# Optimization experiments

Measured on AMD Instinct MI355X. Metric: run time of the kernel, lower is better.

The kernel has to match this reference:

```python
import jax, jax.numpy as jnp
import numpy as np

B, L, D, H, PD = 4, 8192, 512, 8, 1
DK = D // H
EPS = 1e-5


def setup_inputs() -> dict:
    root = jax.random.key(0)
    ks = jax.random.split(root, 16)
    s = 0.02
    inp = {
        'query': jax.random.normal(ks[0], (B, L, D), jnp.float32),
        'key': jax.random.normal(ks[1], (B, L, D), jnp.float32),
        'value': jax.random.normal(ks[2], (B, L, D), jnp.float32),
        'pos': jax.random.uniform(ks[3], (B, L, PD), jnp.float32),
        # QKV projections (xavier-ish small + diagonal init, as in _reset_parameters)
        'Wq': s * jax.random.normal(ks[4], (D, D), jnp.float32) + 0.01 * jnp.eye(D),
        'bq': jnp.zeros((D,), jnp.float32),
        'Wk': s * jax.random.normal(ks[5], (D, D), jnp.float32) + 0.01 * jnp.eye(D),
        'bk': jnp.zeros((D,), jnp.float32),
        'Wv': s * jax.random.normal(ks[6], (D, D), jnp.float32) + 0.01 * jnp.eye(D),
        'bv': jnp.zeros((D,), jnp.float32),
        # per-head LayerNorm affine params for K and V: [H, DK]
        'gK': jnp.ones((H, DK), jnp.float32),
        'betaK': jnp.zeros((H, DK), jnp.float32),
        'gV': jnp.ones((H, DK), jnp.float32),
        'betaV': jnp.zeros((H, DK), jnp.float32),
        # output fc: (D + H*PD) -> D
        'fcW': s * jax.random.normal(ks[7], (D, D + H * PD), jnp.float32),
        'fcb': jnp.zeros((D,), jnp.float32),
    }
    return inp


def _proj(x, W, b):
    # [B,L,D] -> [B,H,L,DK]
    return (x @ W.T + b).reshape(B, L, H, DK).transpose(0, 2, 1, 3)


def _head_layernorm(x, g, b):
    # x: [B,H,L,DK]; per-head affine params g,b: [H,DK]; biased variance (torch LN)
    m = x.mean(-1, keepdims=True)
    v = x.var(-1, keepdims=True)
    xn = (x - m) * jax.lax.rsqrt(v + EPS)
    return xn * g[None, :, None, :] + b[None, :, None, :]


def reference(query, key, value, pos, Wq, bq, Wk, bk, Wv, bv,
              gK, betaK, gV, betaV, fcW, fcb):
    q = _proj(query, Wq, bq)
    k = _proj(key, Wk, bk)
    v = _proj(value, Wv, bv)
    k = _head_layernorm(k, gK, betaK)
    v = _head_layernorm(v, gV, betaV)
    # positional concat: pos [B,L,PD] -> [B,H,L,PD], concat on feature dim
    p = jnp.broadcast_to(pos[:, None, :, :], (B, H, L, PD))
    q = jnp.concatenate([p, q], axis=-1)  # [B,H,L,DK+PD]
    k = jnp.concatenate([p, k], axis=-1)
    v = jnp.concatenate([p, v], axis=-1)
    # Galerkin linear attention: (K^T V)/L then Q @ that
    attn = jnp.einsum('bhld,bhle->bhde', k, v) / L  # [B,H,DK+PD,DK+PD]
    out = jnp.einsum('bhld,bhde->bhle', q, attn)    # [B,H,L,DK+PD]
    out = out.transpose(0, 2, 1, 3).reshape(B, L, H * (DK + PD))
    att_output = out @ fcW.T + fcb  # [B,L,D]
    return (att_output, attn)
```

## Files before the change

kernel.cpp:

```cpp
#include <hip/hip_runtime.h>

typedef __attribute__((ext_vector_type(8))) short short8;
typedef __attribute__((ext_vector_type(4))) float f32x4;
typedef __attribute__((ext_vector_type(4))) unsigned int uint4v;
typedef unsigned short ushort;
typedef unsigned int uint;

#define B_  4
#define L_  8192
#define D_  512
#define H_  8
#define F_  65
#define KVS_ 80
#define EPS_ 1e-5f

__device__ __forceinline__ ushort f2b(float f) {
    uint x = __float_as_uint(f);
    uint r = (x + 0x7FFFu + ((x >> 16) & 1u)) >> 16;
    return (ushort)r;
}
__device__ __forceinline__ float b2f(ushort u) {
    return __uint_as_float(((uint)u) << 16);
}

#define GLD16(gptr, sptr) \
    __builtin_amdgcn_global_load_lds((const __attribute__((address_space(1))) void*)(gptr), \
                                     (__attribute__((address_space(3))) void*)(sptr), 16, 0, 0)


__global__ __launch_bounds__(256)
void cast_w(const float* __restrict__ Wk, const float* __restrict__ Wv,
            ushort* __restrict__ Wb)
{
    const int g = blockIdx.x * 256 + threadIdx.x;
    const int inner = g & 511;
    const int tileIdx = g >> 9;
    const int w   = inner >> 7;
    const int row = inner & 127;
    const int ks  = tileIdx & 15;
    const int nt  = (tileIdx >> 4) & 3;
    const int z   = tileIdx >> 6;
    const float* __restrict__ src = (z == 0) ? Wk : Wv;
    const float* s = &src[(size_t)(nt * 128 + row) * D_ + ks * 32 + w * 8];
    const float4 f0 = *(const float4*)s;
    const float4 f1 = *(const float4*)(s + 4);
    short8 v;
    v[0] = (short)f2b(f0.x); v[1] = (short)f2b(f0.y);
    v[2] = (short)f2b(f0.z); v[3] = (short)f2b(f0.w);
    v[4] = (short)f2b(f1.x); v[5] = (short)f2b(f1.y);
    v[6] = (short)f2b(f1.z); v[7] = (short)f2b(f1.w);
    *(short8*)&Wb[(size_t)tileIdx * 4096 + inner * 8] = v;
}

__global__ __launch_bounds__(512, 2)
void proj_mfma(const float* __restrict__ Xk, const float* __restrict__ Xv,
               const ushort* __restrict__ Wb,
               const float* __restrict__ bk, const float* __restrict__ bv,
               const float* __restrict__ pos,
               const float* __restrict__ gK, const float* __restrict__ betaK,
               const float* __restrict__ gV, const float* __restrict__ betaV,
               ushort* __restrict__ Kh, ushort* __restrict__ Vh)
{
    const int x  = blockIdx.x;
    const int m0 = ((x & 7) * 32 + (x >> 3)) * 128;
    const int z  = blockIdx.y;

    const float* __restrict__ X    = (z == 0) ? Xk : Xv;
    const float* __restrict__ bias = (z == 0) ? bk : bv;

    const int t  = threadIdx.x;
    const int w  = t >> 6, l = t & 63;
    const int wm = (w >> 2) * 64, wn = (w & 3) * 128;
    const int lg = l >> 4, lm = l & 15;

    __shared__ __align__(16) float sAf[2][4096];
    __shared__ __align__(16) short sB[2][16384];

    f32x4 acc[4][8];
#pragma unroll
    for (int i = 0; i < 4; ++i)
#pragma unroll
        for (int j = 0; j < 8; ++j) acc[i][j] = (f32x4){0.f, 0.f, 0.f, 0.f};

    const int lr = l >> 3;
    const int hg = (l & 7) ^ lr;
    const float* ag[2]; int alo[2];
#pragma unroll
    for (int i = 0; i < 2; ++i) {
        const int row = w * 16 + i * 8 + lr;
        ag[i]  = &X[(size_t)(m0 + row) * D_ + hg * 4];
        alo[i] = (w * 2 + i) * 256;
    }

    const ushort* bsrc[4];
#pragma unroll
    for (int nt = 0; nt < 4; ++nt)
        bsrc[nt] = Wb + (size_t)((z * 4 + nt) * 16) * 4096 + t * 8;

    int a0o[4], a1o[4], bro[8];
#pragma unroll
    for (int i = 0; i < 4; ++i) {
        const int r = wm + i * 16 + lm;
        a0o[i] = r * 32 + (((lg * 2)     ^ (r & 7)) * 4);
        a1o[i] = r * 32 + (((lg * 2 + 1) ^ (r & 7)) * 4);
    }
#pragma unroll
    for (int i = 0; i < 8; ++i) {
        const int col = wn + i * 16 + lm;
        bro[i] = (col >> 7) * 4096 + lg * 1024 + (col & 127) * 8;
    }

    auto stage = [&](int ks, int buf) {
#pragma unroll
        for (int i = 0; i < 2; ++i) GLD16(ag[i] + ks * 32, &sAf[buf][alo[i]]);
#pragma unroll
        for (int nt = 0; nt < 4; ++nt)
            GLD16(bsrc[nt] + (size_t)ks * 4096, &sB[buf][nt * 4096 + t * 8]);
    };

    stage(0, 0);
    int cur = 0;
#pragma unroll
    for (int ks = 0; ks < 16; ++ks) {
        __syncthreads();
        if (ks < 15) stage(ks + 1, cur ^ 1);

        short8 af[4], bfv[8];
#pragma unroll
        for (int i = 0; i < 4; ++i) {
            const f32x4 A0 = *(const f32x4*)&sAf[cur][a0o[i]];
            const f32x4 A1 = *(const f32x4*)&sAf[cur][a1o[i]];
            uint u0, u1, u2, u3;
            asm("v_cvt_pk_bf16_f32 %0, %1, %2" : "=v"(u0) : "v"(A0[0]), "v"(A0[1]));
            asm("v_cvt_pk_bf16_f32 %0, %1, %2" : "=v"(u1) : "v"(A0[2]), "v"(A0[3]));
            asm("v_cvt_pk_bf16_f32 %0, %1, %2" : "=v"(u2) : "v"(A1[0]), "v"(A1[1]));
            asm("v_cvt_pk_bf16_f32 %0, %1, %2" : "=v"(u3) : "v"(A1[2]), "v"(A1[3]));
            union { uint4v u4; short8 s8; } cv;
            cv.u4 = (uint4v){u0, u1, u2, u3};
            af[i] = cv.s8;
        }
#pragma unroll
        for (int i = 0; i < 8; ++i) bfv[i] = *(const short8*)&sB[cur][bro[i]];
#pragma unroll
        for (int mt = 0; mt < 4; ++mt)
#pragma unroll
            for (int nt = 0; nt < 8; ++nt)
                acc[mt][nt] = __builtin_amdgcn_mfma_f32_16x16x32_bf16(
                    af[mt], bfv[nt], acc[mt][nt], 0, 0, 0);

        cur ^= 1;
    }

    const int h0 = wn >> 6;
    float bvv[8];
#pragma unroll
    for (int nt = 0; nt < 8; ++nt) bvv[nt] = bias[wn + nt * 16 + lm];

    const float* gp = (z == 0) ? gK : gV;
    const float* bp = (z == 0) ? betaK : betaV;
    ushort* Oh = (z == 0) ? Kh : Vh;
    float gg[8], bb2[8];
#pragma unroll
    for (int nt = 0; nt < 8; ++nt) {
        const int idx = (h0 + (nt >> 2)) * 64 + (nt & 3) * 16 + lm;
        gg[nt]  = gp[idx];
        bb2[nt] = bp[idx];
    }
#pragma unroll
    for (int mt = 0; mt < 4; ++mt) {
#pragma unroll
        for (int r = 0; r < 4; ++r) {
            const int m = m0 + wm + mt * 16 + lg * 4 + r;
            const int bb = m >> 13, ll = m & 8191;
#pragma unroll
            for (int g = 0; g < 2; ++g) {
                const float v0 = acc[mt][g * 4 + 0][r] + bvv[g * 4 + 0];
                const float v1 = acc[mt][g * 4 + 1][r] + bvv[g * 4 + 1];
                const float v2 = acc[mt][g * 4 + 2][r] + bvv[g * 4 + 2];
                const float v3 = acc[mt][g * 4 + 3][r] + bvv[g * 4 + 3];
                float s = v0 + v1 + v2 + v3;
                float q = v0 * v0 + v1 * v1 + v2 * v2 + v3 * v3;
                s += __shfl_xor(s, 1); s += __shfl_xor(s, 2);
                s += __shfl_xor(s, 4); s += __shfl_xor(s, 8);
                q += __shfl_xor(q, 1); q += __shfl_xor(q, 2);
                q += __shfl_xor(q, 4); q += __shfl_xor(q, 8);
                const float mean = s * (1.f / 64.f);
                const float var = q * (1.f / 64.f) - mean * mean;
                const float rs = rsqrtf(var + EPS_);
                const int h = h0 + g;
                ushort* row = Oh + ((size_t)(bb * H_ + h) * L_ + ll) * KVS_;
                row[1 + 0 * 16 + lm] = f2b((v0 - mean) * rs * gg[g * 4 + 0] + bb2[g * 4 + 0]);
                row[1 + 1 * 16 + lm] = f2b((v1 - mean) * rs * gg[g * 4 + 1] + bb2[g * 4 + 1]);
                row[1 + 2 * 16 + lm] = f2b((v2 - mean) * rs * gg[g * 4 + 2] + bb2[g * 4 + 2]);
                row[1 + 3 * 16 + lm] = f2b((v3 - mean) * rs * gg[g * 4 + 3] + bb2[g * 4 + 3]);
                if (lm == 15) row[0] = f2b(pos[m]);
                else          row[F_ + lm] = 0;
            }
        }
    }
}

__global__ __launch_bounds__(256)
void attn_accum(const ushort* __restrict__ Kh, const ushort* __restrict__ Vh,
                float* __restrict__ attn_acc)
{
    const int s = blockIdx.x;
    const int h = blockIdx.y;
    const int b = blockIdx.z;
    const int t = threadIdx.x;

    __shared__ __align__(16) float Ks[64][84];
    __shared__ __align__(16) float Vs[64][84];

    const size_t base = ((size_t)(b * H_ + h) * L_ + s * 512) * KVS_;

    float acc[5][5];
#pragma unroll
    for (int i = 0; i < 5; ++i)
#pragma unroll
        for (int j = 0; j < 5; ++j) acc[i][j] = 0.f;

    const int dg = t / 13, eg = t % 13;
    const bool act = (t < 169);
    const int d0 = dg * 5, e0 = eg * 5;

    for (int c = 0; c < 8; ++c) {
#pragma unroll
        for (int i = 0; i < 3; ++i) {
            const int slot = t + i * 256;
            if (slot < 640) {
                const int r = slot / 10;
                const int cc = (slot - r * 10) * 8;
                const size_t g = base + (size_t)(c * 64 + r) * KVS_ + cc;
                const short8 kv = *(const short8*)(const void*)&Kh[g];
                const short8 vv = *(const short8*)(const void*)&Vh[g];
                float* kd = &Ks[r][cc];
                float* vd = &Vs[r][cc];
#pragma unroll
                for (int e = 0; e < 8; ++e) {
                    kd[e] = b2f((ushort)kv[e]);
                    vd[e] = b2f((ushort)vv[e]);
                }
            }
        }
        __syncthreads();
        if (act) {
#pragma unroll 2
            for (int l = 0; l < 64; ++l) {
                float kf[5], vf[5];
#pragma unroll
                for (int i = 0; i < 5; ++i) kf[i] = Ks[l][d0 + i];
#pragma unroll
                for (int j = 0; j < 5; ++j) vf[j] = Vs[l][e0 + j];
#pragma unroll
                for (int i = 0; i < 5; ++i)
#pragma unroll
                    for (int j = 0; j < 5; ++j)
                        acc[i][j] = fmaf(kf[i], vf[j], acc[i][j]);
            }
        }
        __syncthreads();
    }

    if (act) {
        float* dst = attn_acc + (size_t)(b * H_ + h) * (F_ * F_);
#pragma unroll
        for (int i = 0; i < 5; ++i)
#pragma unroll
            for (int j = 0; j < 5; ++j)
                atomicAdd(&dst[(d0 + i) * F_ + (e0 + j)], acc[i][j]);
    }
}

__global__ __launch_bounds__(256)
void attn_fin(const float* __restrict__ attn_acc, const float* __restrict__ fcW,
              float* __restrict__ attn_out, float* __restrict__ Gq,
              float* __restrict__ gt0)
{
    const int nc = blockIdx.x;
    const int h = blockIdx.y;
    const int b = blockIdx.z;
    const int t = threadIdx.x;

    __shared__ float S[F_][F_];
    __shared__ float Wl[64][F_];

    const float inv = 1.0f / (float)L_;
    const float* __restrict__ src = attn_acc + (size_t)(b * H_ + h) * F_ * F_;
    for (int idx = t; idx < F_ * F_; idx += 256) {
        const float v = src[idx] * inv;
        S[idx / F_][idx % F_] = v;
        if (nc == 0) attn_out[(size_t)(b * H_ + h) * F_ * F_ + idx] = v;
    }
    for (int idx = t; idx < 64 * F_; idx += 256) {
        const int j = idx / F_;
        const int e = idx - j * F_;
        Wl[j][e] = fcW[(size_t)(nc * 64 + j) * (H_ * F_) + h * F_ + e];
    }
    __syncthreads();

    for (int idx = t; idx < F_ * 64; idx += 256) {
        const int d = idx >> 6;
        const int j = idx & 63;
        float g = 0.f;
#pragma unroll 5
        for (int e = 0; e < F_; ++e) g = fmaf(S[d][e], Wl[j][e], g);
        const int n = nc * 64 + j;
        if (d == 0) gt0[((size_t)b * 512 + n) * 8 + h] = g;
        else        Gq[((size_t)b * 512 + n) * 512 + h * 64 + (d - 1)] = g;
    }
}

__global__ __launch_bounds__(256)
void w2_build(const float* __restrict__ Gq, const float* __restrict__ gt0,
              const float* __restrict__ Wq, const float* __restrict__ bq,
              const float* __restrict__ fcb, ushort* __restrict__ W2pk,
              float* __restrict__ Pv, float* __restrict__ C2v)
{
    const int kt  = blockIdx.x;
    const int ntb = blockIdx.y;
    const int b   = blockIdx.z;
    const int t   = threadIdx.x;
    const int n0 = ntb * 64, k0 = kt * 64;

    __shared__ float Sg[64][65];
    __shared__ float Sw[64][65];

    const float* __restrict__ gq = Gq + (size_t)b * 262144;

    float acc[4][4];
#pragma unroll
    for (int i = 0; i < 4; ++i)
#pragma unroll
        for (int j = 0; j < 4; ++j) acc[i][j] = 0.f;
    float c2a[4] = {0.f, 0.f, 0.f, 0.f};

    const int tn = t >> 4, tk = t & 15;

    for (int dc = 0; dc < 8; ++dc) {
        const int d0 = dc * 64;
        for (int idx = t; idx < 4096; idx += 256) {
            const int rr = idx >> 6, cc = idx & 63;
            Sg[rr][cc] = gq[(size_t)(n0 + rr) * 512 + d0 + cc];
            Sw[rr][cc] = Wq[(size_t)(d0 + rr) * 512 + k0 + cc];
        }
        __syncthreads();
        for (int dd = 0; dd < 64; ++dd) {
            float gf[4], wf[4];
#pragma unroll
            for (int i = 0; i < 4; ++i) gf[i] = Sg[tn * 4 + i][dd];
#pragma unroll
            for (int j = 0; j < 4; ++j) wf[j] = Sw[dd][tk * 4 + j];
#pragma unroll
            for (int i = 0; i < 4; ++i)
#pragma unroll
                for (int j = 0; j < 4; ++j)
                    acc[i][j] = fmaf(gf[i], wf[j], acc[i][j]);
        }
        if (tk == 0) {
            for (int dd = 0; dd < 64; ++dd) {
                const float bqv = bq[d0 + dd];
#pragma unroll
                for (int i = 0; i < 4; ++i)
                    c2a[i] = fmaf(bqv, Sg[tn * 4 + i][dd], c2a[i]);
            }
        }
        __syncthreads();
    }

    ushort* wp = W2pk + (size_t)b * 262144;
#pragma unroll
    for (int i = 0; i < 4; ++i)
#pragma unroll
        for (int j = 0; j < 4; ++j) {
            const int n = n0 + tn * 4 + i;
            const int k = k0 + tk * 4 + j;
            wp[(size_t)((n >> 7) * 16 + (k >> 5)) * 4096 +
               ((k >> 3) & 3) * 1024 + (n & 127) * 8 + (k & 7)] = f2b(acc[i][j]);
        }
    if (kt == 0 && tk == 0) {
#pragma unroll
        for (int i = 0; i < 4; ++i) {
            const int n = n0 + tn * 4 + i;
            float p = 0.f;
#pragma unroll
            for (int h = 0; h < 8; ++h) p += gt0[((size_t)b * 512 + n) * 8 + h];
            Pv[b * 512 + n]  = p;
            C2v[b * 512 + n] = fcb[n] + c2a[i];
        }
    }
}

__global__ __launch_bounds__(512, 2)
void out_mfma(const float* __restrict__ query, const ushort* __restrict__ W2pk,
              const float* __restrict__ pos, const float* __restrict__ Pv,
              const float* __restrict__ C2v, float* __restrict__ out)
{
    const int x  = blockIdx.x;
    const int m0 = ((x & 7) * 32 + (x >> 3)) * 128;
    const int b  = m0 >> 13;
    const int t  = threadIdx.x;
    const int w  = t >> 6, l = t & 63;
    const int wm = (w >> 2) * 64, wn = (w & 3) * 128;
    const int lg = l >> 4, lm = l & 15;

    __shared__ __align__(16) float sAf[2][4096];
    __shared__ __align__(16) short sB[2][16384];

    f32x4 acc[4][8];
#pragma unroll
    for (int i = 0; i < 4; ++i)
#pragma unroll
        for (int j = 0; j < 8; ++j) acc[i][j] = (f32x4){0.f, 0.f, 0.f, 0.f};

    const int lr = l >> 3;
    const int hg = (l & 7) ^ lr;
    const float* ag[2]; int alo[2];
#pragma unroll
    for (int i = 0; i < 2; ++i) {
        const int row = w * 16 + i * 8 + lr;
        ag[i]  = &query[(size_t)(m0 + row) * D_ + hg * 4];
        alo[i] = (w * 2 + i) * 256;
    }

    const ushort* bsrc[4];
#pragma unroll
    for (int nt = 0; nt < 4; ++nt)
        bsrc[nt] = W2pk + (size_t)b * 262144 + (size_t)(nt * 16) * 4096 + t * 8;

    int a0o[4], a1o[4], bro[8];
#pragma unroll
    for (int i = 0; i < 4; ++i) {
        const int r = wm + i * 16 + lm;
        a0o[i] = r * 32 + (((lg * 2)     ^ (r & 7)) * 4);
        a1o[i] = r * 32 + (((lg * 2 + 1) ^ (r & 7)) * 4);
    }
#pragma unroll
    for (int i = 0; i < 8; ++i) {
        const int col = wn + i * 16 + lm;
        bro[i] = (col >> 7) * 4096 + lg * 1024 + (col & 127) * 8;
    }

    auto stage = [&](int ks, int buf) {
#pragma unroll
        for (int i = 0; i < 2; ++i) GLD16(ag[i] + ks * 32, &sAf[buf][alo[i]]);
#pragma unroll
        for (int nt = 0; nt < 4; ++nt)
            GLD16(bsrc[nt] + (size_t)ks * 4096, &sB[buf][nt * 4096 + t * 8]);
    };

    stage(0, 0);
    int cur = 0;
#pragma unroll
    for (int ks = 0; ks < 16; ++ks) {
        __syncthreads();
        if (ks < 15) stage(ks + 1, cur ^ 1);

        short8 af[4], bfv[8];
#pragma unroll
        for (int i = 0; i < 4; ++i) {
            const f32x4 A0 = *(const f32x4*)&sAf[cur][a0o[i]];
            const f32x4 A1 = *(const f32x4*)&sAf[cur][a1o[i]];
            uint u0, u1, u2, u3;
            asm("v_cvt_pk_bf16_f32 %0, %1, %2" : "=v"(u0) : "v"(A0[0]), "v"(A0[1]));
            asm("v_cvt_pk_bf16_f32 %0, %1, %2" : "=v"(u1) : "v"(A0[2]), "v"(A0[3]));
            asm("v_cvt_pk_bf16_f32 %0, %1, %2" : "=v"(u2) : "v"(A1[0]), "v"(A1[1]));
            asm("v_cvt_pk_bf16_f32 %0, %1, %2" : "=v"(u3) : "v"(A1[2]), "v"(A1[3]));
            union { uint4v u4; short8 s8; } cv;
            cv.u4 = (uint4v){u0, u1, u2, u3};
            af[i] = cv.s8;
        }
#pragma unroll
        for (int i = 0; i < 8; ++i) bfv[i] = *(const short8*)&sB[cur][bro[i]];
#pragma unroll
        for (int mt = 0; mt < 4; ++mt)
#pragma unroll
            for (int nt = 0; nt < 8; ++nt)
                acc[mt][nt] = __builtin_amdgcn_mfma_f32_16x16x32_bf16(
                    af[mt], bfv[nt], acc[mt][nt], 0, 0, 0);

        cur ^= 1;
    }

    float pv[8], c2[8];
#pragma unroll
    for (int nt = 0; nt < 8; ++nt) {
        const int n = wn + nt * 16 + lm;
        pv[nt] = Pv[b * 512 + n];
        c2[nt] = C2v[b * 512 + n];
    }

#pragma unroll
    for (int mt = 0; mt < 4; ++mt) {
#pragma unroll
        for (int r = 0; r < 4; ++r) {
            const int row = m0 + wm + mt * 16 + lg * 4 + r;
            const float pr = pos[row];
            float* orow = out + (size_t)row * D_;
#pragma unroll
            for (int nt = 0; nt < 8; ++nt)
                orow[wn + nt * 16 + lm] = acc[mt][nt][r] + pr * pv[nt] + c2[nt];
        }
    }
}

extern "C" void kernel_launch(void* const* d_in, const int* in_sizes, int n_in,
                              void* d_out, int out_size, void* d_ws, size_t ws_size,
                              hipStream_t stream)
{
    const float* query = (const float*)d_in[0];
    const float* key   = (const float*)d_in[1];
    const float* value = (const float*)d_in[2];
    const float* pos   = (const float*)d_in[3];
    const float* Wq    = (const float*)d_in[4];
    const float* bq    = (const float*)d_in[5];
    const float* Wk    = (const float*)d_in[6];
    const float* bk    = (const float*)d_in[7];
    const float* Wv    = (const float*)d_in[8];
    const float* bv    = (const float*)d_in[9];
    const float* gK    = (const float*)d_in[10];
    const float* betaK = (const float*)d_in[11];
    const float* gV    = (const float*)d_in[12];
    const float* betaV = (const float*)d_in[13];
    const float* fcW   = (const float*)d_in[14];
    const float* fcb   = (const float*)d_in[15];

    char* ws = (char*)d_ws;
    ushort* Kh       = (ushort*)(ws + 0);
    ushort* Vh       = (ushort*)(ws + 41943040);
    ushort* Wb       = (ushort*)(ws + 83886080);
    float*  attn_acc = (float*) (ws + 84934656);
    float*  Gq       = (float*) (ws + 85479424);
    float*  gt0      = (float*) (ws + 89673728);
    ushort* W2pk     = (ushort*)(ws + 89739264);
    float*  Pv       = (float*) (ws + 91836416);
    float*  C2v      = (float*) (ws + 91844608);

    float* att_out  = (float*)d_out;
    float* attn_out = att_out + 16777216;

    hipMemsetAsync(attn_acc, 0, (size_t)135200 * sizeof(float), stream);

    cast_w<<<dim3(256), 256, 0, stream>>>(Wk, Wv, Wb);

    proj_mfma<<<dim3(256, 2), 512, 0, stream>>>(
        key, value, Wb, bk, bv, pos, gK, betaK, gV, betaV, Kh, Vh);

    attn_accum<<<dim3(16, 8, 4), 256, 0, stream>>>(Kh, Vh, attn_acc);

    attn_fin<<<dim3(8, 8, 4), 256, 0, stream>>>(attn_acc, fcW, attn_out, Gq, gt0);

    w2_build<<<dim3(8, 8, 4), 256, 0, stream>>>(Gq, gt0, Wq, bq, fcb, W2pk, Pv, C2v);

    out_mfma<<<dim3(256), 512, 0, stream>>>(query, W2pk, pos, Pv, C2v, att_out);
}
```

Before: 480.8 us.

## Use bf16 MFMA for K^T V accumulation with partial buffers and reduce kernel

The scalar FMA K^T·V accumulation becomes a bf16 MFMA 16x16x32 kernel. K and V tiles are stored transposed and XOR-swizzled in LDS, and each wave writes its own 80x80 partial sum instead of doing float atomics. A new acc_reduce kernel sums the 32 partials, which removes the memset and atomic contention but adds an extra launch and about 26 MB of partial-buffer traffic. Separately, w2_build's tile loads are vectorized to float4.

After: 411.2 us. 14.5% less time.

```diff
diff --git a/kernel.cpp b/kernel.cpp
--- a/kernel.cpp
+++ b/kernel.cpp
@@ -26,7 +26,6 @@
 #define GLD16(gptr, sptr) \
     __builtin_amdgcn_global_load_lds((const __attribute__((address_space(1))) void*)(gptr), \
                                      (__attribute__((address_space(3))) void*)(sptr), 16, 0, 0)
-
 
 __global__ __launch_bounds__(256)
 void cast_w(const float* __restrict__ Wk, const float* __restrict__ Wv,
@@ -200,75 +199,94 @@
     }
 }
 
-__global__ __launch_bounds__(256)
+__global__ __launch_bounds__(256, 2)
 void attn_accum(const ushort* __restrict__ Kh, const ushort* __restrict__ Vh,
-                float* __restrict__ attn_acc)
+                float* __restrict__ partial)
 {
     const int s = blockIdx.x;
     const int h = blockIdx.y;
     const int b = blockIdx.z;
+    const int bh = b * H_ + h;
     const int t = threadIdx.x;
-
-    __shared__ __align__(16) float Ks[64][84];
-    __shared__ __align__(16) float Vs[64][84];
-
-    const size_t base = ((size_t)(b * H_ + h) * L_ + s * 512) * KVS_;
-
-    float acc[5][5];
+    const int w = t >> 6, l = t & 63;
+    const int lg = l >> 4, lm = l & 15;
+
+    __shared__ __align__(16) short stg[21760];
+    short* KT = stg;
+    short* VT = stg + 10880;
+
+    const size_t base = ((size_t)bh * L_ + (size_t)s * 1024) * KVS_;
+
+    f32x4 acc[5][5];
 #pragma unroll
     for (int i = 0; i < 5; ++i)
 #pragma unroll
-        for (int j = 0; j < 5; ++j) acc[i][j] = 0.f;
-
-    const int dg = t / 13, eg = t % 13;
-    const bool act = (t < 169);
-    const int d0 = dg * 5, e0 = eg * 5;
+        for (int j = 0; j < 5; ++j) acc[i][j] = (f32x4){0.f, 0.f, 0.f, 0.f};
 
     for (int c = 0; c < 8; ++c) {
-#pragma unroll
-        for (int i = 0; i < 3; ++i) {
-            const int slot = t + i * 256;
-            if (slot < 640) {
-                const int r = slot / 10;
-                const int cc = (slot - r * 10) * 8;
-                const size_t g = base + (size_t)(c * 64 + r) * KVS_ + cc;
-                const short8 kv = *(const short8*)(const void*)&Kh[g];
-                const short8 vv = *(const short8*)(const void*)&Vh[g];
-                float* kd = &Ks[r][cc];
-                float* vd = &Vs[r][cc];
-#pragma unroll
-                for (int e = 0; e < 8; ++e) {
-                    kd[e] = b2f((ushort)kv[e]);
-                    vd[e] = b2f((ushort)vv[e]);
-                }
+        __syncthreads();
+#pragma unroll
+        for (int i = 0; i < 5; ++i) {
+            const int g  = t + i * 256;
+            const int lr = g / 10;
+            const int dg = g - lr * 10;
+            const size_t off = base + (size_t)(c * 128 + lr) * KVS_ + dg * 8;
+            const short8 kv = *(const short8*)(const void*)&Kh[off];
+            const short8 vv = *(const short8*)(const void*)&Vh[off];
+            const int lsw = lr ^ ((dg & 7) << 3);
+#pragma unroll
+            for (int j = 0; j < 8; ++j) {
+                KT[(dg * 8 + j) * 136 + lsw] = kv[j];
+                VT[(dg * 8 + j) * 136 + lsw] = vv[j];
             }
         }
         __syncthreads();
-        if (act) {
-#pragma unroll 2
-            for (int l = 0; l < 64; ++l) {
-                float kf[5], vf[5];
-#pragma unroll
-                for (int i = 0; i < 5; ++i) kf[i] = Ks[l][d0 + i];
-#pragma unroll
-                for (int j = 0; j < 5; ++j) vf[j] = Vs[l][e0 + j];
-#pragma unroll
-                for (int i = 0; i < 5; ++i)
-#pragma unroll
-                    for (int j = 0; j < 5; ++j)
-                        acc[i][j] = fmaf(kf[i], vf[j], acc[i][j]);
+
+        const int l0 = w * 32 + lg * 8;
+        short8 Af[5], Bf[5];
+#pragma unroll
+        for (int i = 0; i < 5; ++i) {
+            const int dr = i * 16 + lm;
+            const int sw = ((dr >> 3) & 7) << 3;
+            Af[i] = *(const short8*)&KT[dr * 136 + (l0 ^ sw)];
+            Bf[i] = *(const short8*)&VT[dr * 136 + (l0 ^ sw)];
+        }
+#pragma unroll
+        for (int i = 0; i < 5; ++i)
+#pragma unroll
+            for (int j = 0; j < 5; ++j)
+                acc[i][j] = __builtin_amdgcn_mfma_f32_16x16x32_bf16(
+                    Af[i], Bf[j], acc[i][j], 0, 0, 0);
+    }
+
+    float* dst = partial + ((size_t)(s * 4 + w) * 32 + bh) * 6400;
+#pragma unroll
+    for (int i = 0; i < 5; ++i)
+#pragma unroll
+        for (int j = 0; j < 5; ++j)
+#pragma unroll
+            for (int r = 0; r < 4; ++r) {
+                const int d = i * 16 + lg * 4 + r;
+                const int e = j * 16 + lm;
+                dst[d * 80 + e] = acc[i][j][r];
             }
-        }
-        __syncthreads();
-    }
-
-    if (act) {
-        float* dst = attn_acc + (size_t)(b * H_ + h) * (F_ * F_);
-#pragma unroll
-        for (int i = 0; i < 5; ++i)
-#pragma unroll
-            for (int j = 0; j < 5; ++j)
-                atomicAdd(&dst[(d0 + i) * F_ + (e0 + j)], acc[i][j]);
+}
+
+__global__ __launch_bounds__(256)
+void acc_reduce(const float* __restrict__ partial, float* __restrict__ attn_acc)
+{
+    const int bh = blockIdx.y;
+    const int q  = blockIdx.x;
+    const float4* __restrict__ p4 = (const float4*)partial;
+    float4* __restrict__ o4 = (float4*)attn_acc;
+    for (int i4 = q * 400 + threadIdx.x; i4 < q * 400 + 400; i4 += 256) {
+        float4 s = {0.f, 0.f, 0.f, 0.f};
+#pragma unroll
+        for (int k = 0; k < 32; ++k) {
+            const float4 v = p4[((size_t)k * 32 + bh) * 1600 + i4];
+            s.x += v.x; s.y += v.y; s.z += v.z; s.w += v.w;
+        }
+        o4[(size_t)bh * 1600 + i4] = s;
     }
 }
 
@@ -286,10 +304,11 @@
     __shared__ float Wl[64][F_];
 
     const float inv = 1.0f / (float)L_;
-    const float* __restrict__ src = attn_acc + (size_t)(b * H_ + h) * F_ * F_;
+    const float* __restrict__ src = attn_acc + (size_t)(b * H_ + h) * 6400;
     for (int idx = t; idx < F_ * F_; idx += 256) {
-        const float v = src[idx] * inv;
-        S[idx / F_][idx % F_] = v;
+        const int d = idx / F_, e = idx - d * F_;
+        const float v = src[d * 80 + e] * inv;
+        S[d][e] = v;
         if (nc == 0) attn_out[(size_t)(b * H_ + h) * F_ * F_ + idx] = v;
     }
     for (int idx = t; idx < 64 * F_; idx += 256) {
@@ -339,10 +358,17 @@
 
     for (int dc = 0; dc < 8; ++dc) {
         const int d0 = dc * 64;
-        for (int idx = t; idx < 4096; idx += 256) {
-            const int rr = idx >> 6, cc = idx & 63;
-            Sg[rr][cc] = gq[(size_t)(n0 + rr) * 512 + d0 + cc];
-            Sw[rr][cc] = Wq[(size_t)(d0 + rr) * 512 + k0 + cc];
+#pragma unroll
+        for (int i = 0; i < 4; ++i) {
+            const int idx4 = t + i * 256;
+            const int rr = idx4 >> 4;
+            const int c4 = (idx4 & 15) * 4;
+            const float4 gv = *(const float4*)&gq[(size_t)(n0 + rr) * 512 + d0 + c4];
+            const float4 wv = *(const float4*)&Wq[(size_t)(d0 + rr) * 512 + k0 + c4];
+            Sg[rr][c4] = gv.x; Sg[rr][c4 + 1] = gv.y;
+            Sg[rr][c4 + 2] = gv.z; Sg[rr][c4 + 3] = gv.w;
+            Sw[rr][c4] = wv.x; Sw[rr][c4 + 1] = wv.y;
+            Sw[rr][c4 + 2] = wv.z; Sw[rr][c4 + 3] = wv.w;
         }
         __syncthreads();
         for (int dd = 0; dd < 64; ++dd) {
@@ -530,23 +556,24 @@
     ushort* Vh       = (ushort*)(ws + 41943040);
     ushort* Wb       = (ushort*)(ws + 83886080);
     float*  attn_acc = (float*) (ws + 84934656);
-    float*  Gq       = (float*) (ws + 85479424);
-    float*  gt0      = (float*) (ws + 89673728);
-    ushort* W2pk     = (ushort*)(ws + 89739264);
-    float*  Pv       = (float*) (ws + 91836416);
-    float*  C2v      = (float*) (ws + 91844608);
+    float*  partial  = (float*) (ws + 85753856);
+    float*  Gq       = (float*) (ws + 112307456);
+    float*  gt0      = (float*) (ws + 116501760);
+    ushort* W2pk     = (ushort*)(ws + 116567296);
+    float*  Pv       = (float*) (ws + 118664448);
+    float*  C2v      = (float*) (ws + 118672640);
 
     float* att_out  = (float*)d_out;
     float* attn_out = att_out + 16777216;
 
-    hipMemsetAsync(attn_acc, 0, (size_t)135200 * sizeof(float), stream);
-
     cast_w<<<dim3(256), 256, 0, stream>>>(Wk, Wv, Wb);
 
     proj_mfma<<<dim3(256, 2), 512, 0, stream>>>(
         key, value, Wb, bk, bv, pos, gK, betaK, gV, betaV, Kh, Vh);
 
-    attn_accum<<<dim3(16, 8, 4), 256, 0, stream>>>(Kh, Vh, attn_acc);
+    attn_accum<<<dim3(8, 8, 4), 256, 0, stream>>>(Kh, Vh, partial);
+
+    acc_reduce<<<dim3(4, 32), 256, 0, stream>>>(partial, attn_acc);
 
     attn_fin<<<dim3(8, 8, 4), 256, 0, stream>>>(attn_acc, fcW, attn_out, Gq, gt0);
 
```
